# Performance work log

Measured on AMD Instinct MI355X. Metric: run time of the kernel, lower is better.

## Reference

```python
import jax, jax.numpy as jnp
import numpy as np

CUTOFF_UPPER = 4.5
EYE3 = jnp.eye(3, dtype=jnp.float32)


def tensor_norm(t):
    return (t ** 2).sum((-2, -1))


def decompose_tensor(X):
    # X: [N, C, 3, 3]
    tr_mean = jnp.trace(X, axis1=-2, axis2=-1) / 3.0
    I = tr_mean[..., None, None] * EYE3
    Xt = jnp.swapaxes(X, -2, -1)
    A = 0.5 * (X - Xt)
    S = 0.5 * (X + Xt) - I
    return I, A, S


def chan_linear(T, W, b):
    # torch: Linear applied over the channel axis after permute(0,2,3,1)
    # T: [N, C, 3, 3], W: [C, C], b: [C]
    return jnp.einsum('nkij,ck->ncij', T, W) + b[None, :, None, None]


def setup_inputs() -> dict:
    key = jax.random.key(0)
    ks = jax.random.split(key, 16)
    Np1, H, R, E = 20001, 128, 64, 200000
    X = jax.random.normal(ks[0], (Np1, H, 3, 3), dtype=jnp.float32)
    edge_index = jax.random.randint(ks[1], (2, E), 0, Np1)
    edge_weight = jax.random.uniform(ks[2], (E,), dtype=jnp.float32) * CUTOFF_UPPER
    edge_attr = jax.random.normal(ks[3], (E, R), dtype=jnp.float32)
    s = lambda fin: 1.0 / np.sqrt(fin)
    W1 = jax.random.uniform(ks[4], (3, H, H), minval=-s(H), maxval=s(H), dtype=jnp.float32)
    b1 = jax.random.uniform(ks[5], (3, H), minval=-s(H), maxval=s(H), dtype=jnp.float32)
    W2a = jax.random.uniform(ks[6], (H, R), minval=-s(R), maxval=s(R), dtype=jnp.float32)
    b2a = jax.random.uniform(ks[7], (H,), minval=-s(R), maxval=s(R), dtype=jnp.float32)
    W2b = jax.random.uniform(ks[8], (2 * H, H), minval=-s(H), maxval=s(H), dtype=jnp.float32)
    b2b = jax.random.uniform(ks[9], (2 * H,), minval=-s(H), maxval=s(H), dtype=jnp.float32)
    W2c = jax.random.uniform(ks[10], (3 * H, 2 * H), minval=-s(2 * H), maxval=s(2 * H), dtype=jnp.float32)
    b2c = jax.random.uniform(ks[11], (3 * H,), minval=-s(2 * H), maxval=s(2 * H), dtype=jnp.float32)
    W3 = jax.random.uniform(ks[12], (3, H, H), minval=-s(H), maxval=s(H), dtype=jnp.float32)
    b3 = jax.random.uniform(ks[13], (3, H), minval=-s(H), maxval=s(H), dtype=jnp.float32)
    return dict(X=X, edge_index=edge_index, edge_weight=edge_weight, edge_attr=edge_attr,
                W1=W1, b1=b1, W2a=W2a, b2a=b2a, W2b=W2b, b2b=b2b, W2c=W2c, b2c=b2c, W3=W3, b3=b3)


def reference(X, edge_index, edge_weight, edge_attr, W1, b1, W2a, b2a, W2b, b2b, W2c, b2c, W3, b3):
    Np1, H = X.shape[0], X.shape[1]
    act = jax.nn.silu
    X = X / (tensor_norm(X) + 1.0)[..., None, None]
    I, A, S = decompose_tensor(X)
    I = chan_linear(I, W1[0], b1[0])
    A = chan_linear(A, W1[1], b1[1])
    S = chan_linear(S, W1[2], b1[2])
    Y = I + A + S
    h = act(edge_attr @ W2a.T + b2a)
    h = act(h @ W2b.T + b2b)
    h = act(h @ W2c.T + b2c)  # [E, 3H]
    C = 0.5 * (jnp.cos(edge_weight * (jnp.pi / CUTOFF_UPPER)) + 1.0)
    C = C * (edge_weight < CUTOFF_UPPER).astype(C.dtype)
    ea = (h * C[:, None]).reshape(h.shape[0], H, 3)
    dst, src = edge_index[0], edge_index[1]

    def mp(factor, T):
        msg = factor[:, :, None, None] * T[src]  # [E, H, 3, 3]
        return jax.ops.segment_sum(msg, dst, num_segments=Np1)

    msg = mp(ea[..., 0], I) + mp(ea[..., 1], A) + mp(ea[..., 2], S)
    new_features = jnp.matmul(msg, Y) + jnp.matmul(Y, msg)  # O(3) branch
    I, A, S = decompose_tensor(new_features)
    norm = (tensor_norm(I + A + S) + 1.0)[..., None, None]
    I, A, S = I / norm, A / norm, S / norm
    I = chan_linear(I, W3[0], b3[0])
    A = chan_linear(A, W3[1], b3[1])
    S = chan_linear(S, W3[2], b3[2])
    dX = I + A + S
    return X + dX + jnp.matmul(dX, dX)
```

## Files before the change

### kernel.cpp

```cpp
#include <hip/hip_runtime.h>
#include <math.h>
#include <stdint.h>

typedef unsigned short u16;
typedef __attribute__((ext_vector_type(8))) short short8;
typedef __attribute__((ext_vector_type(4))) float floatx4;

__device__ __forceinline__ float b2f(u16 u){
  union{unsigned int i; float f;} v; v.i = ((unsigned int)u)<<16; return v.f;
}
__device__ __forceinline__ u16 f2b(float f){
  union{unsigned int i; float f;} v; v.f = f;
  unsigned int r = (v.i + 0x7FFFu + ((v.i>>16)&1u))>>16;
  return (u16)r;
}
__device__ __forceinline__ unsigned int pu(u16 lo, u16 hi){
  return (unsigned int)lo | ((unsigned int)hi<<16);
}
__device__ __forceinline__ float gsel(unsigned int u, int s){
  union{unsigned int i; float f;} v;
  v.i = s ? (u & 0xffff0000u) : (u << 16);
  return v.f;
}
__device__ __forceinline__ unsigned int cvtpk(float a, float b){
  unsigned int r;
  asm("v_cvt_pk_bf16_f32 %0, %1, %2" : "=v"(r) : "v"(a), "v"(b));
  return r;
}
__device__ __forceinline__ float fsilu(float t){
  float e = __builtin_amdgcn_exp2f(t * -1.442695040888963f);
  return t * __builtin_amdgcn_rcpf(1.0f + e);
}
__device__ __forceinline__ float ldx(const void* p, size_t i, int isb){
  return isb ? b2f(((const u16*)p)[i]) : ((const float*)p)[i];
}
__device__ __forceinline__ void gll16(const u16* g, u16* l){
  __builtin_amdgcn_global_load_lds(
      (const __attribute__((address_space(1))) unsigned int*)(g),
      (__attribute__((address_space(3))) unsigned int*)(l), 16, 0, 0);
}

__global__ void k_sniff(const void* __restrict__ X, int* __restrict__ flag)
{
  __shared__ int cnt;
  if (threadIdx.x==0) cnt = 0;
  __syncthreads();
  int c = 0;
  for (int t = threadIdx.x; t < 512; t += 256){
    unsigned int u = ((const u16*)X)[2*t];
    int e = (u >> 7) & 0xFF;
    if (e >= 110 && e <= 139) c++;
  }
  atomicAdd(&cnt, c);
  __syncthreads();
  if (threadIdx.x==0) *flag = (cnt > 300) ? 1 : 0;
}

__global__ __launch_bounds__(256) void k_zero_int(int* __restrict__ p, int n)
{
  int i = blockIdx.x*256 + threadIdx.x;
  if (i < n) p[i] = 0;
}

__global__ __launch_bounds__(256) void k_hist(
    const int* __restrict__ ei, int* __restrict__ counts, int E)
{
  int e = blockIdx.x*256 + threadIdx.x;
  if (e < E) atomicAdd(&counts[ei[e]], 1);
}
__global__ __launch_bounds__(256) void k_scan(
    const int* __restrict__ counts, int* __restrict__ rowptr,
    int* __restrict__ fill, int N)
{
  __shared__ int sm[256];
  int tid = threadIdx.x;
  int per = (N + 255) >> 8;
  int lo = tid*per; if (lo > N) lo = N;
  int hi = lo + per; if (hi > N) hi = N;
  int s = 0;
  for (int i = lo; i < hi; i++) s += counts[i];
  sm[tid] = s;
  __syncthreads();
  for (int off=1; off<256; off<<=1){
    int t = (tid >= off) ? sm[tid-off] : 0;
    __syncthreads();
    sm[tid] += t;
    __syncthreads();
  }
  int run = sm[tid] - s;
  for (int i = lo; i < hi; i++){
    int v = counts[i];
    rowptr[i] = run; fill[i] = run;
    run += v;
  }
  if (tid == 0) rowptr[N] = sm[255];
}
__global__ __launch_bounds__(256) void k_scatter(
    const int* __restrict__ ei, int* __restrict__ fill,
    int* __restrict__ eorder, int* __restrict__ srcs, int E)
{
  int e = blockIdx.x*256 + threadIdx.x;
  if (e >= E) return;
  int d = ei[e];
  int pos = atomicAdd(&fill[d], 1);
  eorder[pos] = e;
  srcs[pos] = ei[E + e];
}

__global__ __launch_bounds__(256) void k_cvt_weights(
    const void* __restrict__ W1, const void* __restrict__ W3,
    const void* __restrict__ W2a, const void* __restrict__ W2b,
    const void* __restrict__ W2c, u16* __restrict__ out,
    const int* __restrict__ dflag)
{
  int isb = *dflag;
  int i = blockIdx.x*256 + threadIdx.x;
  if (i >= 237568) return;
  float v;
  if (i < 49152)        v = ldx(W1, i, isb);
  else if (i < 98304)   v = ldx(W3, i-49152, isb);
  else if (i < 106496)  v = ldx(W2a, i-98304, isb);
  else if (i < 139264)  v = ldx(W2b, i-106496, isb);
  else {
    int j = i - 139264;
    int r = j >> 8, c = j & 255;
    v = ldx(W2c, (size_t)((r & 127)*3 + (r >> 7))*256 + c, isb);
  }
  out[i] = f2b(v);
}
__global__ __launch_bounds__(256) void k_cvt_biases(
    const void* __restrict__ b2a, const void* __restrict__ b2b,
    const void* __restrict__ b2c, float* __restrict__ out,
    const int* __restrict__ dflag)
{
  int isb = *dflag;
  int i = blockIdx.x*256 + threadIdx.x;
  if (i < 128) out[i] = ldx(b2a, i, isb);
  else if (i < 384) out[i] = ldx(b2b, i-128, isb);
  else if (i < 768){ int c = i-384; out[i] = ldx(b2c, (c&127)*3 + (c>>7), isb); }
}
__global__ __launch_bounds__(256) void k_perm_eatt(
    const void* __restrict__ eatt, const int* __restrict__ eorder,
    u16* __restrict__ dst, int E, const int* __restrict__ dflag)
{
  int isb = *dflag;
  int row = blockIdx.x*8 + (threadIdx.x >> 5);
  int cp = (threadIdx.x & 31)*2;
  if (row >= E) return;
  int e = eorder[row];
  unsigned int w;
  if (isb){
    w = *(const unsigned int*)((const u16*)eatt + (size_t)e*64 + cp);
  } else {
    float2 v = *(const float2*)((const float*)eatt + (size_t)e*64 + cp);
    w = pu(f2b(v.x), f2b(v.y));
  }
  *(unsigned int*)(dst + (size_t)row*64 + cp) = w;
}

__global__ __launch_bounds__(256) void k_decompose(
    const void* __restrict__ X, u16* __restrict__ Di, u16* __restrict__ Da,
    u16* __restrict__ Ds, int NH, const int* __restrict__ dflag)
{
  __shared__ __align__(16) float buf[4608];
  u16* bufu = (u16*)buf;
  int isb = *dflag;
  int tid = threadIdx.x;
  size_t t0 = (size_t)blockIdx.x*512;
  int validT = (int)((size_t)NH - t0); if (validT > 512) validT = 512;
  int ve = validT*9;
  if (isb){
    const u16* src = (const u16*)X + t0*9;
    for (int idx = tid; idx*8 < ve; idx += 256){
      if (idx*8+7 < ve) ((uint4*)bufu)[idx] = *(const uint4*)(src + idx*8);
      else for (int j=idx*8; j<ve; j++) bufu[j] = src[j];
    }
  } else {
    const float* src = (const float*)X + t0*9;
    for (int idx = tid; idx*4 < ve; idx += 256){
      if (idx*4+3 < ve) ((float4*)buf)[idx] = *(const float4*)(src + idx*4);
      else for (int j=idx*4; j<ve; j++) buf[j] = src[j];
    }
  }
  __syncthreads();
  int pairs = validT >> 1;
  if (tid >= pairs) return;
  int l2 = 2*tid;
  size_t tid2 = t0 + l2;
  int n = (int)(tid2 >> 7), c = (int)(tid2 & 127);
  u16 ri[2], ra[2][3], rs[2][6];
#pragma unroll
  for (int s=0; s<2; s++){
    float x[9]; float nrm = 0.f;
#pragma unroll
    for (int i=0;i<9;i++){
      x[i] = isb ? b2f(bufu[(l2+s)*9+i]) : buf[(l2+s)*9+i];
      nrm += x[i]*x[i];
    }
    float inv = 1.0f/(nrm+1.0f);
#pragma unroll
    for (int i=0;i<9;i++) x[i]*=inv;
    float i0 = (x[0]+x[4]+x[8])*(1.0f/3.0f);
    ri[s] = f2b(i0);
    ra[s][0] = f2b(0.5f*(x[1]-x[3]));
    ra[s][1] = f2b(0.5f*(x[2]-x[6]));
    ra[s][2] = f2b(0.5f*(x[5]-x[7]));
    rs[s][0] = f2b(x[0]-i0);
    rs[s][1] = f2b(0.5f*(x[1]+x[3]));
    rs[s][2] = f2b(0.5f*(x[2]+x[6]));
    rs[s][3] = f2b(x[4]-i0);
    rs[s][4] = f2b(0.5f*(x[5]+x[7]));
    rs[s][5] = f2b(x[8]-i0);
  }
  *(unsigned int*)&Di[tid2] = pu(ri[0], ri[1]);
  size_t ab = ((size_t)n*3)*128 + c;
#pragma unroll
  for (int j=0;j<3;j++)
    *(unsigned int*)&Da[ab + (size_t)j*128] = pu(ra[0][j], ra[1][j]);
  size_t sb = ((size_t)n*6)*128 + c;
#pragma unroll
  for (int j=0;j<6;j++)
    *(unsigned int*)&Ds[sb + (size_t)j*128] = pu(rs[0][j], rs[1][j]);
}

__global__ __launch_bounds__(256) void k_mfma_gemm(
    const u16* __restrict__ A, const u16* __restrict__ B,
    const float* __restrict__ bias, const float* __restrict__ rowscale,
    u16* __restrict__ C, int M, int Ncol, int K, int flags)
{
  __shared__ u16 As[4096];
  __shared__ u16 Bs[4096];
  const int tid = threadIdx.x;
  const int lane = tid & 63, l15 = lane & 15, q = lane >> 4;
  const int wid = tid >> 6, wm = wid & 1, wn = wid >> 1;
  const int n0 = blockIdx.x * 128, m0 = blockIdx.y * 128;

  const int srow = wid*32 + (lane >> 2);
  const int qsrc = (lane & 3) ^ ((lane >> 3) & 3);
  int ar0 = m0 + srow;      if (ar0 >= M) ar0 = M-1;
  int ar1 = m0 + srow + 16; if (ar1 >= M) ar1 = M-1;
  const u16* aSrc0 = A + (size_t)ar0*K + qsrc*8;
  const u16* aSrc1 = A + (size_t)ar1*K + qsrc*8;
  const u16* bSrc0 = B + (size_t)(n0 + srow)*K + qsrc*8;
  const u16* bSrc1 = B + (size_t)(n0 + srow + 16)*K + qsrc*8;
  u16* aDst0 = &As[wid*1024];  u16* aDst1 = &As[wid*1024 + 512];
  u16* bDst0 = &Bs[wid*1024];  u16* bDst1 = &Bs[wid*1024 + 512];

  floatx4 acc[4][4];
#pragma unroll
  for (int i=0;i<4;i++)
#pragma unroll
    for (int j=0;j<4;j++) acc[i][j] = (floatx4)0.f;

  const int qsw  = ((q ^ ((l15 >> 1) & 3)) << 3);
  const int aBase = (wm*64 + l15)*32 + qsw;
  const int bBase = (wn*64 + l15)*32 + qsw;

  for (int k0 = 0; k0 < K; k0 += 32){
    gll16(aSrc0 + k0, aDst0);
    gll16(aSrc1 + k0, aDst1);
    gll16(bSrc0 + k0, bDst0);
    gll16(bSrc1 + k0, bDst1);
    __syncthreads();
    short8 av[4], bv[4];
#pragma unroll
    for (int mt=0; mt<4; mt++)
      av[mt] = *reinterpret_cast<const short8*>(&As[aBase + mt*512]);
#pragma unroll
    for (int nt=0; nt<4; nt++)
      bv[nt] = *reinterpret_cast<const short8*>(&Bs[bBase + nt*512]);
#pragma unroll
    for (int mt=0; mt<4; mt++)
#pragma unroll
      for (int nt=0; nt<4; nt++)
        acc[mt][nt] = __builtin_amdgcn_mfma_f32_16x16x32_bf16(av[mt], bv[nt], acc[mt][nt], 0, 0, 0);
    __syncthreads();
  }

  float biasv[4];
#pragma unroll
  for (int nt=0; nt<4; nt++)
    biasv[nt] = bias ? bias[n0 + wn*64 + nt*16 + l15] : 0.f;
#pragma unroll
  for (int mt=0; mt<4; mt++){
#pragma unroll
    for (int reg=0; reg<4; reg++){
      int row = m0 + wm*64 + mt*16 + q*4 + reg;
      if (row >= M) continue;
      float rs = (flags & 2) ? rowscale[row] : 1.0f;
      float t[4];
#pragma unroll
      for (int nt=0; nt<4; nt++){
        float v = acc[mt][nt][reg] + biasv[nt];
        if (flags & 1) v = fsilu(v);
        t[nt] = v * rs;
      }
      unsigned int p0 = cvtpk(t[0], t[1]);
      unsigned int p1 = cvtpk(t[2], t[3]);
      size_t rb = (size_t)row*Ncol + n0 + wn*64 + l15;
      C[rb]      = (u16)(p0 & 0xffffu);
      C[rb + 16] = (u16)(p0 >> 16);
      C[rb + 32] = (u16)(p1 & 0xffffu);
      C[rb + 48] = (u16)(p1 >> 16);
    }
  }
}

__global__ __launch_bounds__(256) void k_cutoff(
    const void* __restrict__ ew, const int* __restrict__ eorder, int c0,
    float* __restrict__ Cc, int ec, const int* __restrict__ dflag)
{
  int i = blockIdx.x*256 + threadIdx.x;
  if (i >= ec) return;
  int e = eorder[c0 + i];
  float w = ldx(ew, e, *dflag);
  float c = 0.0f;
  if (w < 4.5f) c = 0.5f*(cosf(w*0.6981317007977318f) + 1.0f);
  Cc[i] = c;
}

__global__ __launch_bounds__(128) void k_gather(
    const int* __restrict__ rowptr, const int* __restrict__ srcs,
    int c0, int c1, int first,
    const u16* __restrict__ ea,
    const u16* __restrict__ Pi, const u16* __restrict__ Pa,
    const u16* __restrict__ Ps, const void* __restrict__ b1,
    float* __restrict__ msg, int NH, const int* __restrict__ dflag)
{
  int n = blockIdx.x;
  int lo = rowptr[n], hi = rowptr[n+1];
  if (lo < c0) lo = c0;
  if (hi > c1) hi = c1;
  if (!first && lo >= hi) return;
  int tid = threadIdx.x;
  int slot = tid >> 6;
  int cp = (tid & 63) * 2;
  float m[2][9];
#pragma unroll
  for (int s=0;s<2;s++)
#pragma unroll
    for (int i=0;i<9;i++) m[s][i]=0.f;
  if (lo < hi){
    int isb = *dflag;
    float b0[2], b1v[2], b2v[2];
#pragma unroll
    for (int s=0;s<2;s++){
      b0[s]  = ldx(b1, cp+s,     isb);
      b1v[s] = ldx(b1, 128+cp+s, isb);
      b2v[s] = ldx(b1, 256+cp+s, isb);
    }
    for (int idx = lo + slot; idx < hi; idx += 2){
      int src = srcs[idx];
      const u16* er = ea + (size_t)(idx - c0)*384;
      unsigned int ue0 = *(const unsigned int*)(er + cp);
      unsigned int ue1 = *(const unsigned int*)(er + 128 + cp);
      unsigned int ue2 = *(const unsigned int*)(er + 256 + cp);
      unsigned int upi = *(const unsigned int*)(Pi + (size_t)src*128 + cp);
      size_t ab = (size_t)src*384 + cp;
      unsigned int ua0 = *(const unsigned int*)(Pa + ab);
      unsigned int ua1 = *(const unsigned int*)(Pa + ab + 128);
      unsigned int ua2 = *(const unsigned int*)(Pa + ab + 256);
      size_t sbb = (size_t)src*768 + cp;
      unsigned int us0 = *(const unsigned int*)(Ps + sbb);
      unsigned int us1 = *(const unsigned int*)(Ps + sbb + 128);
      unsigned int us2 = *(const unsigned int*)(Ps + sbb + 256);
      unsigned int us3 = *(const unsigned int*)(Ps + sbb + 384);
      unsigned int us4 = *(const unsigned int*)(Ps + sbb + 512);
      unsigned int us5 = *(const unsigned int*)(Ps + sbb + 640);
#pragma unroll
      for (int s=0;s<2;s++){
        float e0f = gsel(ue0,s), e1f = gsel(ue1,s), e2f = gsel(ue2,s);
        float i1 = gsel(upi,s);
        float a0 = gsel(ua0,s), a1 = gsel(ua1,s), a2 = gsel(ua2,s);
        float s0 = gsel(us0,s), s1 = gsel(us1,s), s2 = gsel(us2,s);
        float s3 = gsel(us3,s), s4 = gsel(us4,s), s5 = gsel(us5,s);
        float bb = e0f*b0[s] + e1f*b1v[s] + e2f*b2v[s];
        float t0 = e0f*i1;
        m[s][0] += t0 + e2f*s0 + bb;
        m[s][1] += e1f*a0 + e2f*s1 + bb;
        m[s][2] += e1f*a1 + e2f*s2 + bb;
        m[s][3] += -e1f*a0 + e2f*s1 + bb;
        m[s][4] += t0 + e2f*s3 + bb;
        m[s][5] += e1f*a2 + e2f*s4 + bb;
        m[s][6] += -e1f*a1 + e2f*s2 + bb;
        m[s][7] += -e1f*a2 + e2f*s4 + bb;
        m[s][8] += t0 + e2f*s5 + bb;
      }
    }
  }
  __shared__ float red[64][18];
  if (slot == 1){
#pragma unroll
    for (int s=0;s<2;s++)
#pragma unroll
      for (int i=0;i<9;i++) red[tid & 63][s*9+i] = m[s][i];
  }
  __syncthreads();
  if (slot == 0){
    int cl = tid & 63;
#pragma unroll
    for (int s=0;s<2;s++)
#pragma unroll
      for (int i=0;i<9;i++) m[s][i] += red[cl][s*9+i];
    size_t o = (size_t)n*128 + cp;
    if (first){
#pragma unroll
      for (int i=0;i<9;i++){
        float2 v = {m[0][i], m[1][i]};
        *(float2*)&msg[(size_t)i*NH + o] = v;
      }
    } else {
#pragma unroll
      for (int i=0;i<9;i++){
        float2* p = (float2*)&msg[(size_t)i*NH + o];
        float2 v = *p;
        v.x += m[0][i]; v.y += m[1][i];
        *p = v;
      }
    }
  }
}

__global__ __launch_bounds__(256) void k_update(
    const float* __restrict__ msg, const u16* __restrict__ Pi,
    const u16* __restrict__ Pa, const u16* __restrict__ Ps,
    const void* __restrict__ b1,
    u16* __restrict__ D2i, u16* __restrict__ D2a, u16* __restrict__ D2s,
    int NH, const int* __restrict__ dflag)
{
  size_t tid2 = ((size_t)blockIdx.x*256 + threadIdx.x)*2;
  if (tid2 >= (size_t)NH) return;
  int isb = *dflag;
  int n = (int)(tid2 >> 7), c = (int)(tid2 & 127);
  float Mx[2][9];
#pragma unroll
  for (int i=0;i<9;i++){
    float2 v = *(const float2*)&msg[(size_t)i*NH + tid2];
    Mx[0][i] = v.x; Mx[1][i] = v.y;
  }
  unsigned int ui = *(const unsigned int*)&Pi[tid2];
  size_t ab = ((size_t)n*3)*128 + c;
  unsigned int ua[3];
#pragma unroll
  for (int j=0;j<3;j++) ua[j] = *(const unsigned int*)&Pa[ab + (size_t)j*128];
  size_t sb = ((size_t)n*6)*128 + c;
  unsigned int us[6];
#pragma unroll
  for (int j=0;j<6;j++) us[j] = *(const unsigned int*)&Ps[sb + (size_t)j*128];
  u16 ri[2], ra[2][3], rs[2][6];
#pragma unroll
  for (int s=0; s<2; s++){
    float i1 = gsel(ui,s);
    float a0 = gsel(ua[0],s), a1 = gsel(ua[1],s), a2 = gsel(ua[2],s);
    float s0 = gsel(us[0],s), s1 = gsel(us[1],s), s2 = gsel(us[2],s);
    float s3 = gsel(us[3],s), s4 = gsel(us[4],s), s5 = gsel(us[5],s);
    float B = ldx(b1,c+s,isb) + ldx(b1,128+c+s,isb) + ldx(b1,256+c+s,isb);
    float Y[9];
    Y[0]= i1+s0+B; Y[1]= a0+s1+B; Y[2]= a1+s2+B;
    Y[3]=-a0+s1+B; Y[4]= i1+s3+B; Y[5]= a2+s4+B;
    Y[6]=-a1+s2+B; Y[7]=-a2+s4+B; Y[8]= i1+s5+B;
    float F[9];
#pragma unroll
    for (int i=0;i<3;i++)
#pragma unroll
      for (int j=0;j<3;j++){
        float acc = 0.f;
#pragma unroll
        for (int t=0;t<3;t++)
          acc += Mx[s][i*3+t]*Y[t*3+j] + Y[i*3+t]*Mx[s][t*3+j];
        F[i*3+j] = acc;
      }
    float nrm = 0.f;
#pragma unroll
    for (int i=0;i<9;i++) nrm += F[i]*F[i];
    float inv = 1.0f/(nrm+1.0f);
    float i2 = (F[0]+F[4]+F[8])*(1.0f/3.0f);
    ri[s] = f2b(i2*inv);
    ra[s][0] = f2b(0.5f*(F[1]-F[3])*inv);
    ra[s][1] = f2b(0.5f*(F[2]-F[6])*inv);
    ra[s][2] = f2b(0.5f*(F[5]-F[7])*inv);
    rs[s][0] = f2b((F[0]-i2)*inv);
    rs[s][1] = f2b(0.5f*(F[1]+F[3])*inv);
    rs[s][2] = f2b(0.5f*(F[2]+F[6])*inv);
    rs[s][3] = f2b((F[4]-i2)*inv);
    rs[s][4] = f2b(0.5f*(F[5]+F[7])*inv);
    rs[s][5] = f2b((F[8]-i2)*inv);
  }
  *(unsigned int*)&D2i[tid2] = pu(ri[0], ri[1]);
#pragma unroll
  for (int j=0;j<3;j++)
    *(unsigned int*)&D2a[ab + (size_t)j*128] = pu(ra[0][j], ra[1][j]);
#pragma unroll
  for (int j=0;j<6;j++)
    *(unsigned int*)&D2s[sb + (size_t)j*128] = pu(rs[0][j], rs[1][j]);
}

__global__ __launch_bounds__(256) void k_final(
    const void* __restrict__ X, const u16* __restrict__ P2i,
    const u16* __restrict__ P2a, const u16* __restrict__ P2s,
    const void* __restrict__ b3, void* __restrict__ out, int NH,
    const int* __restrict__ dflag)
{
  __shared__ __align__(16) float buf[4608];
  u16* bufu = (u16*)buf;
  int isb = *dflag;
  int tid = threadIdx.x;
  size_t t0 = (size_t)blockIdx.x*512;
  int validT = (int)((size_t)NH - t0); if (validT > 512) validT = 512;
  int ve = validT*9;
  if (isb){
    const u16* src = (const u16*)X + t0*9;
    for (int idx = tid; idx*8 < ve; idx += 256){
      if (idx*8+7 < ve) ((uint4*)bufu)[idx] = *(const uint4*)(src + idx*8);
      else for (int j=idx*8; j<ve; j++) bufu[j] = src[j];
    }
  } else {
    const float* src = (const float*)X + t0*9;
    for (int idx = tid; idx*4 < ve; idx += 256){
      if (idx*4+3 < ve) ((float4*)buf)[idx] = *(const float4*)(src + idx*4);
      else for (int j=idx*4; j<ve; j++) buf[j] = src[j];
    }
  }
  __syncthreads();
  int pairs = validT >> 1;
  int l2 = 2*tid;
  size_t tid2 = t0 + l2;
  float vout[2][9];
  if (tid < pairs){
    int n = (int)(tid2 >> 7), c = (int)(tid2 & 127);
    unsigned int ui = *(const unsigned int*)&P2i[tid2];
    size_t ab = ((size_t)n*3)*128 + c;
    unsigned int ua[3];
#pragma unroll
    for (int j=0;j<3;j++) ua[j] = *(const unsigned int*)&P2a[ab + (size_t)j*128];
    size_t sb = ((size_t)n*6)*128 + c;
    unsigned int us[6];
#pragma unroll
    for (int j=0;j<6;j++) us[j] = *(const unsigned int*)&P2s[sb + (size_t)j*128];
#pragma unroll
    for (int s=0; s<2; s++){
      float i1 = gsel(ui,s);
      float a0 = gsel(ua[0],s), a1 = gsel(ua[1],s), a2 = gsel(ua[2],s);
      float s0 = gsel(us[0],s), s1 = gsel(us[1],s), s2 = gsel(us[2],s);
      float s3 = gsel(us[3],s), s4 = gsel(us[4],s), s5 = gsel(us[5],s);
      float B = ldx(b3,c+s,isb) + ldx(b3,128+c+s,isb) + ldx(b3,256+c+s,isb);
      float dX[9];
      dX[0]= i1+s0+B; dX[1]= a0+s1+B; dX[2]= a1+s2+B;
      dX[3]=-a0+s1+B; dX[4]= i1+s3+B; dX[5]= a2+s4+B;
      dX[6]=-a1+s2+B; dX[7]=-a2+s4+B; dX[8]= i1+s5+B;
      float x[9]; float nrm = 0.f;
#pragma unroll
      for (int i=0;i<9;i++){
        x[i] = isb ? b2f(bufu[(l2+s)*9+i]) : buf[(l2+s)*9+i];
        nrm += x[i]*x[i];
      }
      float inv = 1.0f/(nrm+1.0f);
#pragma unroll
      for (int i=0;i<3;i++)
#pragma unroll
        for (int j=0;j<3;j++){
          float acc = 0.f;
#pragma unroll
          for (int t=0;t<3;t++) acc += dX[i*3+t]*dX[t*3+j];
          vout[s][i*3+j] = x[i*3+j]*inv + dX[i*3+j] + acc;
        }
    }
  }
  __syncthreads();
  if (tid < pairs){
    if (isb){
#pragma unroll
      for (int s=0;s<2;s++)
#pragma unroll
        for (int i=0;i<9;i++) bufu[(l2+s)*9+i] = f2b(vout[s][i]);
    } else {
#pragma unroll
      for (int s=0;s<2;s++)
#pragma unroll
        for (int i=0;i<9;i++) buf[(l2+s)*9+i] = vout[s][i];
    }
  }
  __syncthreads();
  if (isb){
    u16* dst = (u16*)out + t0*9;
    for (int idx = tid; idx*8 < ve; idx += 256){
      if (idx*8+7 < ve) *(uint4*)(dst + idx*8) = ((const uint4*)bufu)[idx];
      else for (int j=idx*8; j<ve; j++) dst[j] = bufu[j];
    }
  } else {
    float* dst = (float*)out + t0*9;
    for (int idx = tid; idx*4 < ve; idx += 256){
      if (idx*4+3 < ve) *(float4*)(dst + idx*4) = ((const float4*)buf)[idx];
      else for (int j=idx*4; j<ve; j++) dst[j] = buf[j];
    }
  }
}

extern "C" void kernel_launch(void* const* d_in, const int* in_sizes, int n_in,
                              void* d_out, int out_size, void* d_ws, size_t ws_size,
                              hipStream_t stream)
{
  const void* X    = d_in[0];
  const int*  ei   = (const int*)d_in[1];
  const void* ew   = d_in[2];
  const void* eatt = d_in[3];
  const void* W1   = d_in[4];
  const void* b1   = d_in[5];
  const void* W2a  = d_in[6];
  const void* b2a  = d_in[7];
  const void* W2b  = d_in[8];
  const void* b2b  = d_in[9];
  const void* W2c  = d_in[10];
  const void* b2c  = d_in[11];
  const void* W3   = d_in[12];
  const void* b3   = d_in[13];

  const int NH = in_sizes[0]/9;
  const int E  = in_sizes[2];
  const int N  = NH/128;

  auto aln = [](size_t x){ return (x + 255) & ~(size_t)255; };
  char* ws = (char*)d_ws;
  size_t off = 0;
  size_t o_flag = off; off += 256;
  size_t o_msg  = off; off += aln((size_t)NH*9*4);
  size_t o_Di   = off; off += aln((size_t)NH*2);
  size_t o_Da   = off; off += aln((size_t)NH*6);
  size_t o_Ds   = off; off += aln((size_t)NH*12);
  size_t o_Pi   = off; off += aln((size_t)NH*2);
  size_t o_Pa   = off; off += aln((size_t)NH*6);
  size_t o_Ps   = off; off += aln((size_t)NH*12);
  size_t o_cnt  = off; off += aln((size_t)N*4);
  size_t o_rp   = off; off += aln((size_t)(N+1)*4);
  size_t o_fill = off; off += aln((size_t)N*4);
  size_t o_eord = off; off += aln((size_t)E*4);
  size_t o_srcs = off; off += aln((size_t)E*4);
  size_t o_eattb= off; off += aln((size_t)E*64*2);
  size_t o_wb   = off; off += aln((size_t)237568*2);
  size_t o_bf   = off; off += aln((size_t)768*4);
  size_t persistent = off;

  int EC;
  {
    size_t avail = (ws_size > persistent + 4096) ? (ws_size - persistent - 4096) : 0;
    size_t ecmax = avail / 1540;
    if (ecmax > (size_t)E) ecmax = (size_t)E;
    EC = (int)(ecmax & ~(size_t)1023);
    if (EC < 1024) EC = 1024;
  }
  size_t o_h1 = persistent;
  size_t o_h2 = o_h1 + aln((size_t)EC*256);
  size_t o_ea = o_h2 + aln((size_t)EC*512);
  size_t o_Cc = o_ea + aln((size_t)EC*768);
  (void)n_in; (void)out_size;

  int* dflag = (int*)(ws + o_flag);
  u16* Di = (u16*)(ws + o_Di);
  u16* Da = (u16*)(ws + o_Da);
  u16* Ds = (u16*)(ws + o_Ds);
  u16* Pi = (u16*)(ws + o_Pi);
  u16* Pa = (u16*)(ws + o_Pa);
  u16* Ps = (u16*)(ws + o_Ps);
  float* msg = (float*)(ws + o_msg);
  int* counts = (int*)(ws + o_cnt);
  int* rowptr = (int*)(ws + o_rp);
  int* fill   = (int*)(ws + o_fill);
  int* eorder = (int*)(ws + o_eord);
  int* srcs   = (int*)(ws + o_srcs);
  u16* eattb  = (u16*)(ws + o_eattb);
  u16* wb     = (u16*)(ws + o_wb);
  float* bf   = (float*)(ws + o_bf);
  u16* h1 = (u16*)(ws + o_h1);
  u16* h2 = (u16*)(ws + o_h2);
  u16* ea = (u16*)(ws + o_ea);
  float* Cc = (float*)(ws + o_Cc);

  dim3 blk(256);
  auto gemm = [&](const u16* A, const u16* Bw, const float* bias, const float* rs,
                  u16* C, int M, int Ncol, int K, int flags){
    dim3 grid(Ncol/128, (M+127)/128);
    k_mfma_gemm<<<grid, blk, 0, stream>>>(A, Bw, bias, rs, C, M, Ncol, K, flags);
  };

  k_sniff<<<1, blk, 0, stream>>>(X, dflag);
  k_cvt_weights<<<(237568+255)/256, blk, 0, stream>>>(W1, W3, W2a, W2b, W2c, wb, dflag);
  k_cvt_biases<<<3, blk, 0, stream>>>(b2a, b2b, b2c, bf, dflag);
  k_decompose<<<(NH+511)/512, blk, 0, stream>>>(X, Di, Da, Ds, NH, dflag);
  gemm(Di, wb,       nullptr, nullptr, Pi, N,   128, 128, 0);
  gemm(Da, wb+16384, nullptr, nullptr, Pa, 3*N, 128, 128, 0);
  gemm(Ds, wb+32768, nullptr, nullptr, Ps, 6*N, 128, 128, 0);
  k_zero_int<<<(N+255)/256, blk, 0, stream>>>(counts, N);
  k_hist<<<(E+255)/256, blk, 0, stream>>>(ei, counts, E);
  k_scan<<<1, blk, 0, stream>>>(counts, rowptr, fill, N);
  k_scatter<<<(E+255)/256, blk, 0, stream>>>(ei, fill, eorder, srcs, E);
  k_perm_eatt<<<(E+7)/8, blk, 0, stream>>>(eatt, eorder, eattb, E, dflag);
  for (int c0 = 0; c0 < E; c0 += EC){
    int ec = E - c0; if (ec > EC) ec = EC;
    k_cutoff<<<(ec+255)/256, blk, 0, stream>>>(ew, eorder, c0, Cc, ec, dflag);
    gemm(eattb + (size_t)c0*64, wb+98304,  bf,     nullptr, h1, ec, 128, 64,  1);
    gemm(h1,                    wb+106496, bf+128, nullptr, h2, ec, 256, 128, 1);
    gemm(h2,                    wb+139264, bf+384, Cc,      ea, ec, 384, 256, 1|2);
    k_gather<<<N, dim3(128), 0, stream>>>(rowptr, srcs, c0, c0+ec,
                                          (c0==0)?1:0,
                                          ea, Pi, Pa, Ps, b1, msg, NH, dflag);
  }
  k_update<<<(NH/2+255)/256, blk, 0, stream>>>(msg, Pi, Pa, Ps, b1, Di, Da, Ds, NH, dflag);
  gemm(Di, wb+49152, nullptr, nullptr, Pi, N,   128, 128, 0);
  gemm(Da, wb+65536, nullptr, nullptr, Pa, 3*N, 128, 128, 0);
  gemm(Ds, wb+81920, nullptr, nullptr, Ps, 6*N, 128, 128, 0);
  k_final<<<(NH+511)/512, blk, 0, stream>>>(X, Pi, Pa, Ps, b3, d_out, NH, dflag);
}
```

Baseline: 829.9 us.

## Fuse three-layer edge MLP into one kernel keeping activations in LDS

Replaces the three separate edge-MLP GEMM launches with a single kernel that computes all three layers for a 128-edge tile, keeping the intermediate h1/h2 activations in shared memory instead of writing them to and reading them from global memory. The workspace no longer reserves h1/h2 buffers, so the edge chunk size can grow and fewer chunk iterations are needed. The cost is about 120KB of LDS per block, which limits occupancy to one block per CU, and weight tiles are reloaded with a sync on every k-step without double buffering.

```diff
diff --git a/kernel.cpp b/kernel.cpp
--- a/kernel.cpp
+++ b/kernel.cpp
@@ -303,6 +303,188 @@
       C[rb + 32] = (u16)(p1 & 0xffffu);
       C[rb + 48] = (u16)(p1 >> 16);
     }
+  }
+}
+
+__global__ __launch_bounds__(256) void k_edge_mlp(
+    const u16* __restrict__ eatt,
+    const u16* __restrict__ Wa,
+    const u16* __restrict__ Wb,
+    const u16* __restrict__ Wc,
+    const float* __restrict__ bias,
+    const float* __restrict__ Cc,
+    u16* __restrict__ ea, int ec)
+{
+  __shared__ u16 lds[61440];
+  u16* Ain = lds;
+  u16* H1  = lds + 8192;
+  u16* H2  = lds + 24576;
+  u16* Bs  = lds + 57344;
+  const int tid = threadIdx.x;
+  const int lane = tid & 63, l15 = lane & 15, q = lane >> 4;
+  const int wid = tid >> 6, wm = wid & 1, wn = wid >> 1;
+  const int r0 = blockIdx.x * 128;
+
+  const int srow = wid*32 + (lane >> 2);
+  const int qsrc = (lane & 3) ^ ((lane >> 3) & 3);
+  const int qsw  = ((q ^ ((l15 >> 1) & 3)) << 3);
+  const int aBase = (wm*64 + l15)*32 + qsw;
+  const int bBase = (wn*64 + l15)*32 + qsw;
+
+  {
+    int er0 = r0 + srow;      if (er0 >= ec) er0 = ec-1;
+    int er1 = r0 + srow + 16; if (er1 >= ec) er1 = ec-1;
+    const u16* s0 = eatt + (size_t)er0*64 + qsrc*8;
+    const u16* s1 = eatt + (size_t)er1*64 + qsrc*8;
+    gll16(s0,      Ain + wid*1024);
+    gll16(s1,      Ain + wid*1024 + 512);
+    gll16(s0 + 32, Ain + 4096 + wid*1024);
+    gll16(s1 + 32, Ain + 4096 + wid*1024 + 512);
+  }
+
+  floatx4 acc[4][4];
+  short8 av[4], bv[4];
+
+#pragma unroll
+  for (int i=0;i<4;i++)
+#pragma unroll
+    for (int j=0;j<4;j++) acc[i][j] = (floatx4)0.f;
+#pragma unroll
+  for (int ks=0; ks<2; ks++){
+    const u16* w0 = Wa + (size_t)srow*64 + ks*32 + qsrc*8;
+    gll16(w0,        Bs + wid*1024);
+    gll16(w0 + 16*64, Bs + wid*1024 + 512);
+    __syncthreads();
+    const u16* At = Ain + ks*4096;
+#pragma unroll
+    for (int mt=0; mt<4; mt++)
+      av[mt] = *reinterpret_cast<const short8*>(&At[aBase + mt*512]);
+#pragma unroll
+    for (int nt=0; nt<4; nt++)
+      bv[nt] = *reinterpret_cast<const short8*>(&Bs[bBase + nt*512]);
+#pragma unroll
+    for (int mt=0; mt<4; mt++)
+#pragma unroll
+      for (int nt=0; nt<4; nt++)
+        acc[mt][nt] = __builtin_amdgcn_mfma_f32_16x16x32_bf16(av[mt], bv[nt], acc[mt][nt], 0, 0, 0);
+    __syncthreads();
+  }
+  {
+    float biasv[4];
+#pragma unroll
+    for (int nt=0; nt<4; nt++)
+      biasv[nt] = bias[wn*64 + nt*16 + l15];
+#pragma unroll
+    for (int mt=0; mt<4; mt++)
+#pragma unroll
+      for (int reg=0; reg<4; reg++){
+        int row = wm*64 + mt*16 + q*4 + reg;
+        int rsw = ((q*4+reg) >> 1) & 3;
+#pragma unroll
+        for (int nt=0; nt<4; nt++){
+          int col = wn*64 + nt*16 + l15;
+          float v = fsilu(acc[mt][nt][reg] + biasv[nt]);
+          int ks = col >> 5, g = (col>>3)&3, e = col&7;
+          H1[ks*4096 + row*32 + ((g ^ rsw)<<3) + e] = f2b(v);
+        }
+      }
+  }
+
+#pragma unroll
+  for (int cb=0; cb<2; cb++){
+#pragma unroll
+    for (int i=0;i<4;i++)
+#pragma unroll
+      for (int j=0;j<4;j++) acc[i][j] = (floatx4)0.f;
+#pragma unroll
+    for (int ks=0; ks<4; ks++){
+      const u16* w0 = Wb + (size_t)(cb*128 + srow)*128 + ks*32 + qsrc*8;
+      gll16(w0,         Bs + wid*1024);
+      gll16(w0 + 16*128, Bs + wid*1024 + 512);
+      __syncthreads();
+      const u16* At = H1 + ks*4096;
+#pragma unroll
+      for (int mt=0; mt<4; mt++)
+        av[mt] = *reinterpret_cast<const short8*>(&At[aBase + mt*512]);
+#pragma unroll
+      for (int nt=0; nt<4; nt++)
+        bv[nt] = *reinterpret_cast<const short8*>(&Bs[bBase + nt*512]);
+#pragma unroll
+      for (int mt=0; mt<4; mt++)
+#pragma unroll
+        for (int nt=0; nt<4; nt++)
+          acc[mt][nt] = __builtin_amdgcn_mfma_f32_16x16x32_bf16(av[mt], bv[nt], acc[mt][nt], 0, 0, 0);
+      __syncthreads();
+    }
+    float biasv[4];
+#pragma unroll
+    for (int nt=0; nt<4; nt++)
+      biasv[nt] = bias[128 + cb*128 + wn*64 + nt*16 + l15];
+#pragma unroll
+    for (int mt=0; mt<4; mt++)
+#pragma unroll
+      for (int reg=0; reg<4; reg++){
+        int row = wm*64 + mt*16 + q*4 + reg;
+        int rsw = ((q*4+reg) >> 1) & 3;
+#pragma unroll
+        for (int nt=0; nt<4; nt++){
+          int col = cb*128 + wn*64 + nt*16 + l15;
+          float v = fsilu(acc[mt][nt][reg] + biasv[nt]);
+          int ks = col >> 5, g = (col>>3)&3, e = col&7;
+          H2[ks*4096 + row*32 + ((g ^ rsw)<<3) + e] = f2b(v);
+        }
+      }
+  }
+
+#pragma unroll
+  for (int cb=0; cb<3; cb++){
+#pragma unroll
+    for (int i=0;i<4;i++)
+#pragma unroll
+      for (int j=0;j<4;j++) acc[i][j] = (floatx4)0.f;
+#pragma unroll
+    for (int ks=0; ks<8; ks++){
+      const u16* w0 = Wc + (size_t)(cb*128 + srow)*256 + ks*32 + qsrc*8;
+      gll16(w0,         Bs + wid*1024);
+      gll16(w0 + 16*256, Bs + wid*1024 + 512);
+      __syncthreads();
+      const u16* At = H2 + ks*4096;
+#pragma unroll
+      for (int mt=0; mt<4; mt++)
+        av[mt] = *reinterpret_cast<const short8*>(&At[aBase + mt*512]);
+#pragma unroll
+      for (int nt=0; nt<4; nt++)
+        bv[nt] = *reinterpret_cast<const short8*>(&Bs[bBase + nt*512]);
+#pragma unroll
+      for (int mt=0; mt<4; mt++)
+#pragma unroll
+        for (int nt=0; nt<4; nt++)
+          acc[mt][nt] = __builtin_amdgcn_mfma_f32_16x16x32_bf16(av[mt], bv[nt], acc[mt][nt], 0, 0, 0);
+      __syncthreads();
+    }
+    float biasv[4];
+#pragma unroll
+    for (int nt=0; nt<4; nt++)
+      biasv[nt] = bias[384 + cb*128 + wn*64 + nt*16 + l15];
+#pragma unroll
+    for (int mt=0; mt<4; mt++)
+#pragma unroll
+      for (int reg=0; reg<4; reg++){
+        int row = r0 + wm*64 + mt*16 + q*4 + reg;
+        if (row >= ec) continue;
+        float rs = Cc[row];
+        float t[4];
+#pragma unroll
+        for (int nt=0; nt<4; nt++)
+          t[nt] = fsilu(acc[mt][nt][reg] + biasv[nt]) * rs;
+        unsigned int p0 = cvtpk(t[0], t[1]);
+        unsigned int p1 = cvtpk(t[2], t[3]);
+        size_t rb = (size_t)row*384 + cb*128 + wn*64 + l15;
+        ea[rb]      = (u16)(p0 & 0xffffu);
+        ea[rb + 16] = (u16)(p0 >> 16);
+        ea[rb + 32] = (u16)(p1 & 0xffffu);
+        ea[rb + 48] = (u16)(p1 >> 16);
+      }
   }
 }
 
@@ -643,14 +825,12 @@
   int EC;
   {
     size_t avail = (ws_size > persistent + 4096) ? (ws_size - persistent - 4096) : 0;
-    size_t ecmax = avail / 1540;
+    size_t ecmax = avail / 772;
     if (ecmax > (size_t)E) ecmax = (size_t)E;
     EC = (int)(ecmax & ~(size_t)1023);
     if (EC < 1024) EC = 1024;
   }
-  size_t o_h1 = persistent;
-  size_t o_h2 = o_h1 + aln((size_t)EC*256);
-  size_t o_ea = o_h2 + aln((size_t)EC*512);
+  size_t o_ea = persistent;
   size_t o_Cc = o_ea + aln((size_t)EC*768);
   (void)n_in; (void)out_size;
 
@@ -670,8 +850,6 @@
   u16* eattb  = (u16*)(ws + o_eattb);
   u16* wb     = (u16*)(ws + o_wb);
   float* bf   = (float*)(ws + o_bf);
-  u16* h1 = (u16*)(ws + o_h1);
-  u16* h2 = (u16*)(ws + o_h2);
   u16* ea = (u16*)(ws + o_ea);
   float* Cc = (float*)(ws + o_Cc);
 
@@ -697,9 +875,8 @@
   for (int c0 = 0; c0 < E; c0 += EC){
     int ec = E - c0; if (ec > EC) ec = EC;
     k_cutoff<<<(ec+255)/256, blk, 0, stream>>>(ew, eorder, c0, Cc, ec, dflag);
-    gemm(eattb + (size_t)c0*64, wb+98304,  bf,     nullptr, h1, ec, 128, 64,  1);
-    gemm(h1,                    wb+106496, bf+128, nullptr, h2, ec, 256, 128, 1);
-    gemm(h2,                    wb+139264, bf+384, Cc,      ea, ec, 384, 256, 1|2);
+    k_edge_mlp<<<(ec+127)/128, blk, 0, stream>>>(
+        eattb + (size_t)c0*64, wb+98304, wb+106496, wb+139264, bf, Cc, ea, ec);
     k_gather<<<N, dim3(128), 0, stream>>>(rowptr, srcs, c0, c0+ec,
                                           (c0==0)?1:0,
                                           ea, Pi, Pa, Ps, b1, msg, NH, dflag);
```

After: 808.5 us. -2.6%, faster.
